# Optimization experiments

Hardware: AMD Instinct MI355X
Metric: run time of the kernel (lower is better)

## Reference

```python
import jax, jax.numpy as jnp
import numpy as np

B, S, F_IN = 128, 64, 32          # batch, window_size (seq), input features
E, L, H, HOR = 96, 4, 8, 24       # embed_dim, num_layers, num_heads, horizon
E2 = 2 * E                        # attention hidden size (conv output channels)
D = E2 // H                       # head_dim
FLAT = S * E2                     # flattened fc feature size


def _ln(x, scale, offset, eps=1e-5):
    mu = jnp.mean(x, axis=-1, keepdims=True)
    var = jnp.var(x, axis=-1, keepdims=True)
    return (x - mu) * jax.lax.rsqrt(var + eps) * scale + offset


def _gattention(h, qk_w, qk_b, mass_w, mass_b, v_w, v_b):
    b, s, _ = h.shape
    qk = (h @ qk_w + qk_b).reshape(b, s, H, D).transpose(0, 2, 1, 3)  # (b,h,s,d)
    # d^2 = |qi|^2 + |qj|^2 - 2 qi.qj  (GEMM identity; exact value is >= 0)
    sq = jnp.sum(qk * qk, axis=-1)                                    # (b,h,s)
    dot = jnp.einsum('bhid,bhjd->bhij', qk, qk)
    d2 = jnp.maximum(sq[:, :, :, None] + sq[:, :, None, :] - 2.0 * dot, 0.0) + 1e-6
    mass = jax.nn.softplus(h @ mass_w + mass_b).transpose(0, 2, 1)    # (b,h,s)
    scores = (mass[:, :, :, None] * mass[:, :, None, :]) / d2
    w = jax.nn.softmax(scores, axis=-1)
    v = (h @ v_w + v_b).reshape(b, s, H, D).transpose(0, 2, 1, 3)
    out = jnp.einsum('bhij,bhjd->bhid', w, v)
    return out.transpose(0, 2, 1, 3).reshape(b, s, E2)


def setup_inputs() -> dict:
    key = jax.random.key(0)
    ks = iter(jax.random.split(key, 16))
    r = lambda *shape: jax.random.normal(next(ks), shape, jnp.float32) * 0.02
    return dict(
        x=jax.random.normal(next(ks), (B, S, F_IN), jnp.float32),
        proj_w=r(F_IN, E), proj_b=jnp.zeros((E,), jnp.float32),
        ln0_s=jnp.ones((E,), jnp.float32), ln0_o=jnp.zeros((E,), jnp.float32),
        conv_w=r(4, 4, E, E2), conv_b=jnp.zeros((E2,), jnp.float32),
        ln1_s=jnp.ones((E2,), jnp.float32), ln1_o=jnp.zeros((E2,), jnp.float32),
        qk_w=r(L, E2, E2), qk_b=jnp.zeros((L, E2), jnp.float32),
        mass_w=r(L, E2, H), mass_b=jnp.zeros((L, H), jnp.float32),
        v_w=r(L, E2, E2), v_b=jnp.zeros((L, E2), jnp.float32),
        norm_s=jnp.ones((L, E2), jnp.float32), norm_o=jnp.zeros((L, E2), jnp.float32),
        mlp_w1=r(E2, 4 * E), mlp_b1=jnp.zeros((4 * E,), jnp.float32),
        mlp_w2=r(4 * E, E2), mlp_b2=jnp.zeros((E2,), jnp.float32),
        fc_w=r(FLAT, FLAT), fc_b=jnp.zeros((FLAT,), jnp.float32),
        ln2_s=jnp.ones((FLAT,), jnp.float32), ln2_o=jnp.zeros((FLAT,), jnp.float32),
        out_w=r(FLAT, HOR), out_b=jnp.zeros((HOR,), jnp.float32),
    )


def reference(x, proj_w, proj_b, ln0_s, ln0_o, conv_w, conv_b, ln1_s, ln1_o,
              qk_w, qk_b, mass_w, mass_b, v_w, v_b, norm_s, norm_o,
              mlp_w1, mlp_b1, mlp_w2, mlp_b2, fc_w, fc_b, ln2_s, ln2_o,
              out_w, out_b):
    # proj: Linear -> LN -> gelu
    h = jax.nn.gelu(_ln(x @ proj_w + proj_b, ln0_s, ln0_o))            # (B,S,E)
    # hk.Conv2D on rank-3 input: treated as a single unbatched HWC image
    y = jax.lax.conv_general_dilated(
        h[None], conv_w, window_strides=(1, 1), padding='SAME',
        dimension_numbers=('NHWC', 'HWIO', 'NHWC'))[0] + conv_b        # (B,S,E2)
    h = jax.nn.gelu(_ln(y, ln1_s, ln1_o))
    for i in range(L):
        a = _gattention(h, qk_w[i], qk_b[i], mass_w[i], mass_b[i], v_w[i], v_b[i])
        h = jax.nn.gelu(_ln(h + a, norm_s[i], norm_o[i]))
    h = h + (jax.nn.gelu(h @ mlp_w1 + mlp_b1) @ mlp_w2 + mlp_b2)
    f = _ln(jax.nn.gelu(h.reshape(B, FLAT) @ fc_w + fc_b), ln2_s, ln2_o)
    return f @ out_w + out_b                                           # (B,HOR)
```

## Files before the change

kernel.cpp:

```cpp
#include <hip/hip_runtime.h>
#include <math.h>

typedef __attribute__((ext_vector_type(8))) short short8;
typedef __attribute__((ext_vector_type(4))) float f32x4;

__device__ __forceinline__ unsigned short bf16_rne(float f) {
  union { float f; unsigned u; } x; x.f = f;
  unsigned r = x.u + 0x7FFFu + ((x.u >> 16) & 1u);
  return (unsigned short)(r >> 16);
}

__device__ __forceinline__ float gelu_f(float x) {
  float z = 0.7978845608028654f * (x + 0.044715f * x * x * x);
  z = fminf(fmaxf(z, -15.f), 15.f);
  float e = __expf(2.f * z);
  float th = (e - 1.f) / (e + 1.f);
  return 0.5f * x * (1.f + th);
}

__device__ __forceinline__ float softplus_f(float x) {
  return (x > 15.f) ? x : log1pf(__expf(x));
}

__device__ __forceinline__ float wave_sum(float v) {
  #pragma unroll
  for (int off = 32; off > 0; off >>= 1) v += __shfl_down(v, off, 64);
  return v;
}

__global__ __launch_bounds__(256) void pre_kern(
    const float* __restrict__ x, const float* __restrict__ w,
    const float* __restrict__ b, const float* __restrict__ s,
    const float* __restrict__ o, unsigned short* __restrict__ h0bf,
    const float* __restrict__ cw, unsigned short* __restrict__ cwT)
{
  if (blockIdx.x >= 2048) {
    int e = (blockIdx.x - 2048) * 256 + threadIdx.x;
    int co = e % 192, rest = e / 192;
    int ci = rest % 96, tap = rest / 96;
    cwT[((size_t)tap * 192 + co) * 96 + ci] = bf16_rne(cw[e]);
    return;
  }
  int t = threadIdx.x, wave = t >> 6, l = t & 63;
  size_t row = (size_t)blockIdx.x * 4 + wave;
  const float* xr = x + row * 32;
  bool has2 = (l < 32);
  int c1 = l, c2 = has2 ? 64 + l : 0;
  float v1 = b[c1], v2 = b[c2];
  #pragma unroll
  for (int k = 0; k < 32; ++k) {
    float xv = xr[k];
    v1 += xv * w[k * 96 + c1];
    v2 += xv * w[k * 96 + c2];
  }
  if (!has2) v2 = 0.f;
  float sum = wave_sum(v1 + v2);
  float ssq = wave_sum(v1 * v1 + v2 * v2);
  sum = __shfl(sum, 0, 64); ssq = __shfl(ssq, 0, 64);
  float mu = sum / 96.f, var = ssq / 96.f - mu * mu;
  float inv = rsqrtf(var + 1e-5f);
  float f1 = gelu_f((v1 - mu) * inv * s[c1] + o[c1]);
  h0bf[row * 96 + c1] = bf16_rne(f1);
  if (has2) {
    float f2 = gelu_f((v2 - mu) * inv * s[c2] + o[c2]);
    h0bf[row * 96 + c2] = bf16_rne(f2);
  }
}

__global__ __launch_bounds__(256) void conv_kern(
    const unsigned short* __restrict__ h0bf, const unsigned short* __restrict__ cwT,
    const float* __restrict__ cb, float* __restrict__ y)
{
  __shared__ unsigned short As[12 * 64 * 8];
  __shared__ unsigned short Ws[12 * 64 * 8];
  int t = threadIdx.x;
  int i = blockIdx.x;
  int n0 = blockIdx.y * 64;
  int wave = t >> 6, lane = t & 63, quad = lane >> 4, l16 = lane & 15;
  f32x4 zero4 = {0.f, 0.f, 0.f, 0.f};
  f32x4 acc[4];
  #pragma unroll
  for (int nt = 0; nt < 4; ++nt) acc[nt] = zero4;
  for (int tap = 0; tap < 16; ++tap) {
    int kh = tap >> 2, kw = tap & 3;
    int si = i + kh - 1;
    if (si < 0 || si >= 128) continue;
    {
      int j = t & 63, g = t >> 6;
      int sj = j + kw - 1;
      bool ok = (sj >= 0 && sj < 64);
      #pragma unroll
      for (int q = 0; q < 3; ++q) {
        int kb = g + 4 * q;
        short8 v = {0,0,0,0,0,0,0,0};
        if (ok) v = *(const short8*)(h0bf + (size_t)(si * 64 + sj) * 96 + kb * 8);
        *(short8*)(As + (kb * 64 + j) * 8) = v;
      }
    }
    {
      int n = t & 63, g = t >> 6;
      #pragma unroll
      for (int q = 0; q < 3; ++q) {
        int kb = g + 4 * q;
        *(short8*)(Ws + (kb * 64 + n) * 8) =
            *(const short8*)(cwT + ((size_t)tap * 192 + n0 + n) * 96 + kb * 8);
      }
    }
    __syncthreads();
    #pragma unroll
    for (int ks = 0; ks < 3; ++ks) {
      int kbq = ks * 4 + quad;
      short8 a = *(const short8*)(As + (kbq * 64 + wave * 16 + l16) * 8);
      #pragma unroll
      for (int nt = 0; nt < 4; ++nt) {
        short8 b = *(const short8*)(Ws + (kbq * 64 + nt * 16 + l16) * 8);
        acc[nt] = __builtin_amdgcn_mfma_f32_16x16x32_bf16(a, b, acc[nt], 0, 0, 0);
      }
    }
    __syncthreads();
  }
  #pragma unroll
  for (int nt = 0; nt < 4; ++nt) {
    int col = n0 + nt * 16 + l16;
    float bv = cb[col];
    #pragma unroll
    for (int r = 0; r < 4; ++r) {
      int row = wave * 16 + quad * 4 + r;
      y[(size_t)(i * 64 + row) * 192 + col] = acc[nt][r] + bv;
    }
  }
}

__global__ __launch_bounds__(256) void ln_act_kern(
    const float* __restrict__ y, const float* __restrict__ res,
    const float* __restrict__ s, const float* __restrict__ o,
    float* __restrict__ h32, unsigned short* __restrict__ hbf)
{
  int t = threadIdx.x, wave = t >> 6, l = t & 63;
  size_t base = ((size_t)blockIdx.x * 4 + wave) * 192;
  float v0 = y[base + l], v1 = y[base + 64 + l], v2 = y[base + 128 + l];
  if (res) { v0 += res[base + l]; v1 += res[base + 64 + l]; v2 += res[base + 128 + l]; }
  float sum = wave_sum(v0 + v1 + v2);
  float ssq = wave_sum(v0 * v0 + v1 * v1 + v2 * v2);
  sum = __shfl(sum, 0, 64); ssq = __shfl(ssq, 0, 64);
  float mu = sum * (1.f / 192.f);
  float var = ssq * (1.f / 192.f) - mu * mu;
  float inv = rsqrtf(var + 1e-5f);
  float f0 = gelu_f((v0 - mu) * inv * s[l] + o[l]);
  float f1 = gelu_f((v1 - mu) * inv * s[64 + l] + o[64 + l]);
  float f2 = gelu_f((v2 - mu) * inv * s[128 + l] + o[128 + l]);
  h32[base + l] = f0; h32[base + 64 + l] = f1; h32[base + 128 + l] = f2;
  hbf[base + l] = bf16_rne(f0); hbf[base + 64 + l] = bf16_rne(f1); hbf[base + 128 + l] = bf16_rne(f2);
}

__device__ __forceinline__ void stage_w(
    unsigned short* Wt, const float* qw, const float* vw, const float* mw,
    int half, int k0, int t)
{
  for (int c = t; c < 1664; c += 256) {
    int kb = c / 208, n = c - kb * 208;
    short8 v8;
    if (n < 192) {
      const float* src = (n < 96) ? (qw + half * 96 + n) : (vw + half * 96 + n - 96);
      #pragma unroll
      for (int jj = 0; jj < 8; ++jj)
        v8[jj] = (short)bf16_rne(src[(size_t)(k0 + kb * 8 + jj) * 192]);
    } else if (n < 196) {
      const float* src = mw + half * 4 + (n - 192);
      #pragma unroll
      for (int jj = 0; jj < 8; ++jj)
        v8[jj] = (short)bf16_rne(src[(size_t)(k0 + kb * 8 + jj) * 8]);
    } else {
      v8 = (short8){0,0,0,0,0,0,0,0};
    }
    *(short8*)(Wt + c * 8) = v8;
  }
}

__global__ __launch_bounds__(256) void layer_attn(
    const unsigned short* __restrict__ hbf,
    const float* __restrict__ qw, const float* __restrict__ qb,
    const float* __restrict__ vw, const float* __restrict__ vb,
    const float* __restrict__ mw, const float* __restrict__ mb,
    float* __restrict__ att)
{
  extern __shared__ char smem[];
  unsigned short* qk_lds = (unsigned short*)smem;
  unsigned short* v_ldsp = (unsigned short*)(smem + 16384);
  unsigned short* w_bfp  = (unsigned short*)(smem + 32768);
  float* mmp = (float*)(smem + 65536);
  float* sqp = (float*)(smem + 66560);
  unsigned short* A_bf = (unsigned short*)smem;
  unsigned short* Wt   = (unsigned short*)(smem + 24576);

  int t = threadIdx.x;
  int bb = blockIdx.x >> 1, half = blockIdx.x & 1;
  int wv = t >> 6, lane = t & 63, quad = lane >> 4, l16 = lane & 15;

  for (int c = t; c < 1536; c += 256) {
    int kb = c >> 6, m = c & 63;
    *(short8*)(A_bf + c * 8) =
        *(const short8*)(hbf + ((size_t)bb * 64 + m) * 192 + kb * 8);
  }
  stage_w(Wt, qw, vw, mw, half, 0, t);
  __syncthreads();
  f32x4 acc[13];
  #pragma unroll
  for (int i = 0; i < 13; ++i) acc[i] = (f32x4){0.f,0.f,0.f,0.f};
  for (int kt = 0; kt < 3; ++kt) {
    #pragma unroll
    for (int ks = 0; ks < 2; ++ks) {
      int kq = ks * 4 + quad;
      short8 a = *(const short8*)(A_bf + ((kt * 8 + kq) * 64 + wv * 16 + l16) * 8);
      #pragma unroll
      for (int nt = 0; nt < 13; ++nt) {
        short8 b = *(const short8*)(Wt + (kq * 208 + nt * 16 + l16) * 8);
        acc[nt] = __builtin_amdgcn_mfma_f32_16x16x32_bf16(a, b, acc[nt], 0, 0, 0);
      }
    }
    if (kt < 2) {
      __syncthreads();
      stage_w(Wt, qw, vw, mw, half, (kt + 1) * 64, t);
      __syncthreads();
    }
  }
  __syncthreads();

  {
    int zh = t >> 6, zs = t & 63;
    *(short8*)(qk_lds + ((zh * 4 + 3) * 64 + zs) * 8) = (short8){0,0,0,0,0,0,0,0};
  }
  int row = wv * 16 + quad * 4;
  #pragma unroll
  for (int nt = 0; nt < 6; ++nt) {
    int n = nt * 16 + l16;
    int hl = n / 24, d = n - hl * 24;
    float bqv = qb[half * 96 + n];
    #pragma unroll
    for (int r = 0; r < 4; ++r)
      qk_lds[((hl * 4 + (d >> 3)) * 64 + row + r) * 8 + (d & 7)] =
          bf16_rne(acc[nt][r] + bqv);
  }
  #pragma unroll
  for (int nt = 0; nt < 6; ++nt) {
    int n = nt * 16 + l16;
    int hl = n / 24, d = n - hl * 24;
    float bvv = vb[half * 96 + n];
    #pragma unroll
    for (int r = 0; r < 4; ++r) {
      int sidx = row + r;
      v_ldsp[((hl * 8 + (sidx >> 3)) * 32 + d) * 8 + (sidx & 7)] =
          bf16_rne(acc[nt + 6][r] + bvv);
    }
  }
  if (l16 < 4) {
    float mbv = mb[half * 4 + l16];
    #pragma unroll
    for (int r = 0; r < 4; ++r)
      mmp[(row + r) * 4 + l16] = softplus_f(acc[12][r] + mbv);
  }
  __syncthreads();

  const unsigned short* qh = qk_lds + (wv * 4) * 64 * 8;
  short8 frag[4];
  #pragma unroll
  for (int x2 = 0; x2 < 4; ++x2)
    frag[x2] = *(const short8*)(qh + (quad * 64 + x2 * 16 + l16) * 8);
  f32x4 s16[4][4];
  #pragma unroll
  for (int mt = 0; mt < 4; ++mt)
    #pragma unroll
    for (int nt = 0; nt < 4; ++nt)
      s16[mt][nt] = __builtin_amdgcn_mfma_f32_16x16x32_bf16(
          frag[mt], frag[nt], (f32x4){0.f,0.f,0.f,0.f}, 0, 0, 0);
  float* sqh = sqp + wv * 64;
  #pragma unroll
  for (int mt = 0; mt < 4; ++mt)
    #pragma unroll
    for (int r = 0; r < 4; ++r)
      if (l16 == quad * 4 + r) sqh[mt * 16 + l16] = s16[mt][mt][r];
  __syncthreads();
  f32x4 sqr[4], mr[4];
  float sqc[4], mc[4];
  #pragma unroll
  for (int mt = 0; mt < 4; ++mt) {
    sqr[mt] = *(const f32x4*)(sqh + mt * 16 + quad * 4);
    #pragma unroll
    for (int r = 0; r < 4; ++r) mr[mt][r] = mmp[(mt * 16 + quad * 4 + r) * 4 + wv];
  }
  #pragma unroll
  for (int nt = 0; nt < 4; ++nt) {
    sqc[nt] = sqh[nt * 16 + l16];
    mc[nt]  = mmp[(nt * 16 + l16) * 4 + wv];
  }
  #pragma unroll
  for (int mt = 0; mt < 4; ++mt)
    #pragma unroll
    for (int nt = 0; nt < 4; ++nt)
      #pragma unroll
      for (int r = 0; r < 4; ++r) {
        float d2 = fmaxf(sqr[mt][r] + sqc[nt] - 2.f * s16[mt][nt][r], 0.f) + 1e-6f;
        s16[mt][nt][r] = mr[mt][r] * mc[nt] / d2;
      }
  f32x4 inv4[4];
  #pragma unroll
  for (int mt = 0; mt < 4; ++mt)
    #pragma unroll
    for (int r = 0; r < 4; ++r) {
      float mx = fmaxf(fmaxf(s16[mt][0][r], s16[mt][1][r]),
                       fmaxf(s16[mt][2][r], s16[mt][3][r]));
      #pragma unroll
      for (int off = 1; off < 16; off <<= 1) mx = fmaxf(mx, __shfl_xor(mx, off, 64));
      float sm = 0.f;
      #pragma unroll
      for (int nt = 0; nt < 4; ++nt) {
        float e = __expf(s16[mt][nt][r] - mx);
        s16[mt][nt][r] = e;
        sm += e;
      }
      #pragma unroll
      for (int off = 1; off < 16; off <<= 1) sm += __shfl_xor(sm, off, 64);
      inv4[mt][r] = 1.f / sm;
    }

  unsigned short* wb = w_bfp + wv * (8 * 64 * 8);
  #pragma unroll
  for (int mt = 0; mt < 4; ++mt)
    #pragma unroll
    for (int nt = 0; nt < 4; ++nt)
      #pragma unroll
      for (int r = 0; r < 4; ++r) {
        int si = mt * 16 + quad * 4 + r, sj = nt * 16 + l16;
        wb[((sj >> 3) * 64 + si) * 8 + (sj & 7)] = bf16_rne(s16[mt][nt][r]);
      }
  __syncthreads();

  const unsigned short* vh = v_ldsp + wv * (8 * 32 * 8);
  f32x4 o2[4][2];
  #pragma unroll
  for (int mt = 0; mt < 4; ++mt)
    #pragma unroll
    for (int nt = 0; nt < 2; ++nt) o2[mt][nt] = (f32x4){0.f,0.f,0.f,0.f};
  #pragma unroll
  for (int ks = 0; ks < 2; ++ks) {
    int kq = ks * 4 + quad;
    short8 aw[4], bv2[2];
    #pragma unroll
    for (int mt = 0; mt < 4; ++mt)
      aw[mt] = *(const short8*)(wb + (kq * 64 + mt * 16 + l16) * 8);
    #pragma unroll
    for (int nt = 0; nt < 2; ++nt)
      bv2[nt] = *(const short8*)(vh + (kq * 32 + nt * 16 + l16) * 8);
    #pragma unroll
    for (int mt = 0; mt < 4; ++mt)
      #pragma unroll
      for (int nt = 0; nt < 2; ++nt)
        o2[mt][nt] = __builtin_amdgcn_mfma_f32_16x16x32_bf16(aw[mt], bv2[nt], o2[mt][nt], 0, 0, 0);
  }
  int hg = half * 4 + wv;
  size_t obase = ((size_t)bb * 64) * 192 + hg * 24;
  #pragma unroll
  for (int mt = 0; mt < 4; ++mt)
    #pragma unroll
    for (int nt = 0; nt < 2; ++nt) {
      int col = nt * 16 + l16;
      if (col < 24) {
        #pragma unroll
        for (int r = 0; r < 4; ++r) {
          int sidx = mt * 16 + quad * 4 + r;
          att[obase + (size_t)sidx * 192 + col] = o2[mt][nt][r] * inv4[mt][r];
        }
      }
    }
}

__global__ __launch_bounds__(256) void gemm_small(
    const unsigned short* __restrict__ A, int lda,
    const float* __restrict__ W, int ldw,
    const float* __restrict__ bias, const float* __restrict__ res,
    float* __restrict__ outF, unsigned short* __restrict__ outB,
    int K, int ldo, int act)
{
  __shared__ unsigned short As[8 * 64 * 8];
  __shared__ unsigned short Ws[8 * 64 * 8];
  int t = threadIdx.x;
  int m0 = blockIdx.x * 64, n0 = blockIdx.y * 64;
  int wave = t >> 6, lane = t & 63, quad = lane >> 4, l16 = lane & 15;
  f32x4 zero4 = {0.f, 0.f, 0.f, 0.f};
  f32x4 acc[4];
  #pragma unroll
  for (int nt = 0; nt < 4; ++nt) acc[nt] = zero4;
  for (int k0 = 0; k0 < K; k0 += 64) {
    {
      int kb = t & 7, m = t >> 3;
      #pragma unroll
      for (int r = 0; r < 2; ++r) {
        int mm = m + r * 32;
        *(short8*)(As + (kb * 64 + mm) * 8) =
            *(const short8*)(A + (size_t)(m0 + mm) * lda + k0 + kb * 8);
      }
    }
    {
      int n = t & 63, g = t >> 6;
      #pragma unroll
      for (int q = 0; q < 2; ++q) {
        int kb = g + 4 * q;
        short8 v;
        #pragma unroll
        for (int jj = 0; jj < 8; ++jj)
          v[jj] = (short)bf16_rne(W[(size_t)(k0 + kb * 8 + jj) * ldw + n0 + n]);
        *(short8*)(Ws + (kb * 64 + n) * 8) = v;
      }
    }
    __syncthreads();
    #pragma unroll
    for (int ks = 0; ks < 2; ++ks) {
      short8 a = *(const short8*)(As + ((ks * 4 + quad) * 64 + wave * 16 + l16) * 8);
      #pragma unroll
      for (int nt = 0; nt < 4; ++nt) {
        short8 b = *(const short8*)(Ws + ((ks * 4 + quad) * 64 + nt * 16 + l16) * 8);
        acc[nt] = __builtin_amdgcn_mfma_f32_16x16x32_bf16(a, b, acc[nt], 0, 0, 0);
      }
    }
    __syncthreads();
  }
  #pragma unroll
  for (int nt = 0; nt < 4; ++nt) {
    int col = n0 + nt * 16 + l16;
    float bv = bias[col];
    #pragma unroll
    for (int r = 0; r < 4; ++r) {
      int row = m0 + wave * 16 + quad * 4 + r;
      float v = acc[nt][r] + bv;
      if (act) v = gelu_f(v);
      if (res) v += res[(size_t)row * ldo + col];
      if (outF) outF[(size_t)row * ldo + col] = v;
      if (outB) outB[(size_t)row * ldo + col] = bf16_rne(v);
    }
  }
}

__global__ __launch_bounds__(256) void gemm_fc(
    const unsigned short* __restrict__ A, const float* __restrict__ W,
    float* __restrict__ part)
{
  __shared__ unsigned short As[8 * 128 * 8];
  __shared__ unsigned short Bs[8 * 64 * 8];
  int t = threadIdx.x;
  int n0 = blockIdx.x * 64;
  int split = blockIdx.y;
  int wave = t >> 6, lane = t & 63, quad = lane >> 4, l16 = lane & 15;
  int wm = wave * 32;
  int a_kb = t & 7, a_m = t >> 3;
  int w_n4 = t & 15, w_kr = t >> 4;
  f32x4 zero4 = {0.f, 0.f, 0.f, 0.f};
  f32x4 acc[2][4];
  #pragma unroll
  for (int mt = 0; mt < 2; ++mt)
    #pragma unroll
    for (int nt = 0; nt < 4; ++nt) acc[mt][nt] = zero4;
  int kk = split * 3072;
  short8 aR[4]; f32x4 wR[4];
  #pragma unroll
  for (int r = 0; r < 4; ++r)
    aR[r] = *(const short8*)(A + (size_t)(a_m + r * 32) * 12288 + kk + a_kb * 8);
  #pragma unroll
  for (int r = 0; r < 4; ++r)
    wR[r] = *(const f32x4*)(W + (size_t)(kk + w_kr + 16 * r) * 12288 + n0 + w_n4 * 4);
  for (int it = 0; it < 48; ++it) {
    #pragma unroll
    for (int r = 0; r < 4; ++r)
      *(short8*)(As + (a_kb * 128 + a_m + r * 32) * 8) = aR[r];
    #pragma unroll
    for (int r = 0; r < 4; ++r) {
      int k = w_kr + 16 * r, kb = k >> 3, kj = k & 7;
      #pragma unroll
      for (int j = 0; j < 4; ++j)
        Bs[(kb * 64 + w_n4 * 4 + j) * 8 + kj] = bf16_rne(wR[r][j]);
    }
    __syncthreads();
    if (it < 47) {
      int kn = kk + 64;
      #pragma unroll
      for (int r = 0; r < 4; ++r)
        aR[r] = *(const short8*)(A + (size_t)(a_m + r * 32) * 12288 + kn + a_kb * 8);
      #pragma unroll
      for (int r = 0; r < 4; ++r)
        wR[r] = *(const f32x4*)(W + (size_t)(kn + w_kr + 16 * r) * 12288 + n0 + w_n4 * 4);
    }
    #pragma unroll
    for (int ks = 0; ks < 2; ++ks) {
      int kq = ks * 4 + quad;
      short8 a[2], b[4];
      #pragma unroll
      for (int mt = 0; mt < 2; ++mt)
        a[mt] = *(const short8*)(As + (kq * 128 + wm + mt * 16 + l16) * 8);
      #pragma unroll
      for (int nt = 0; nt < 4; ++nt)
        b[nt] = *(const short8*)(Bs + (kq * 64 + nt * 16 + l16) * 8);
      #pragma unroll
      for (int mt = 0; mt < 2; ++mt)
        #pragma unroll
        for (int nt = 0; nt < 4; ++nt)
          acc[mt][nt] = __builtin_amdgcn_mfma_f32_16x16x32_bf16(a[mt], b[nt], acc[mt][nt], 0, 0, 0);
    }
    __syncthreads();
    kk += 64;
  }
  float* po = part + (size_t)split * 128 * 12288;
  #pragma unroll
  for (int mt = 0; mt < 2; ++mt) {
    #pragma unroll
    for (int nt = 0; nt < 4; ++nt) {
      int col = n0 + nt * 16 + l16;
      #pragma unroll
      for (int r = 0; r < 4; ++r) {
        int row = wm + mt * 16 + quad * 4 + r;
        po[(size_t)row * 12288 + col] = acc[mt][nt][r];
      }
    }
  }
}

__global__ __launch_bounds__(256) void final_kern(
    const float* __restrict__ part, const float* __restrict__ fb,
    const float* __restrict__ s, const float* __restrict__ o,
    const float* __restrict__ ow, const float* __restrict__ ob,
    float* __restrict__ out)
{
  __shared__ float gls[12288];
  __shared__ float a1[4], a2[4];
  __shared__ float red[4][24];
  int m = blockIdx.x, t = threadIdx.x;
  const f32x4* p0 = (const f32x4*)(part + (size_t)m * 12288);
  const size_t S4 = (size_t)128 * 12288 / 4;
  float s1 = 0.f, s2 = 0.f;
  for (int k4 = t; k4 < 3072; k4 += 256) {
    f32x4 v = p0[k4] + p0[k4 + S4] + p0[k4 + 2 * S4] + p0[k4 + 3 * S4];
    f32x4 bb = *(const f32x4*)(fb + k4 * 4);
    f32x4 g;
    #pragma unroll
    for (int c = 0; c < 4; ++c) g[c] = gelu_f(v[c] + bb[c]);
    *(f32x4*)(gls + k4 * 4) = g;
    s1 += g[0] + g[1] + g[2] + g[3];
    s2 += g[0]*g[0] + g[1]*g[1] + g[2]*g[2] + g[3]*g[3];
  }
  s1 = wave_sum(s1); s2 = wave_sum(s2);
  int wv = t >> 6, ln = t & 63;
  if (ln == 0) { a1[wv] = s1; a2[wv] = s2; }
  __syncthreads();
  float sum = a1[0] + a1[1] + a1[2] + a1[3];
  float ssq = a2[0] + a2[1] + a2[2] + a2[3];
  float mu = sum / 12288.f, var = ssq / 12288.f - mu * mu;
  float inv = rsqrtf(var + 1e-5f);
  f32x4 acc6[6];
  #pragma unroll
  for (int j = 0; j < 6; ++j) acc6[j] = (f32x4){0.f,0.f,0.f,0.f};
  for (int k = t; k < 12288; k += 256) {
    float f = (gls[k] - mu) * inv * s[k] + o[k];
    const f32x4* owr = (const f32x4*)(ow + (size_t)k * 24);
    #pragma unroll
    for (int j = 0; j < 6; ++j) acc6[j] += f * owr[j];
  }
  #pragma unroll
  for (int j = 0; j < 6; ++j)
    #pragma unroll
    for (int c = 0; c < 4; ++c) {
      float v = wave_sum(acc6[j][c]);
      if (ln == 0) red[wv][j * 4 + c] = v;
    }
  __syncthreads();
  if (t < 24) out[m * 24 + t] = red[0][t] + red[1][t] + red[2][t] + red[3][t] + ob[t];
}

extern "C" void kernel_launch(void* const* d_in, const int* in_sizes, int n_in,
                              void* d_out, int out_size, void* d_ws, size_t ws_size,
                              hipStream_t stream) {
  const float* x      = (const float*)d_in[0];
  const float* proj_w = (const float*)d_in[1];
  const float* proj_b = (const float*)d_in[2];
  const float* ln0_s  = (const float*)d_in[3];
  const float* ln0_o  = (const float*)d_in[4];
  const float* conv_w = (const float*)d_in[5];
  const float* conv_b = (const float*)d_in[6];
  const float* ln1_s  = (const float*)d_in[7];
  const float* ln1_o  = (const float*)d_in[8];
  const float* qk_w   = (const float*)d_in[9];
  const float* qk_b   = (const float*)d_in[10];
  const float* mass_w = (const float*)d_in[11];
  const float* mass_b = (const float*)d_in[12];
  const float* v_w    = (const float*)d_in[13];
  const float* v_b    = (const float*)d_in[14];
  const float* norm_s = (const float*)d_in[15];
  const float* norm_o = (const float*)d_in[16];
  const float* mlp_w1 = (const float*)d_in[17];
  const float* mlp_b1 = (const float*)d_in[18];
  const float* mlp_w2 = (const float*)d_in[19];
  const float* mlp_b2 = (const float*)d_in[20];
  const float* fc_w   = (const float*)d_in[21];
  const float* fc_b   = (const float*)d_in[22];
  const float* ln2_s  = (const float*)d_in[23];
  const float* ln2_o  = (const float*)d_in[24];
  const float* out_w  = (const float*)d_in[25];
  const float* out_b  = (const float*)d_in[26];
  float* out = (float*)d_out;

  char* ws = (char*)d_ws;
  unsigned short* h0bf = (unsigned short*)(ws + 0);
  float* h32           = (float*)(ws + 1572864);
  unsigned short* hbf  = (unsigned short*)(ws + 7864320);
  unsigned short* cwT  = (unsigned short*)(ws + 11010048);
  char* sc = ws + 11599872;
  float* t_att = (float*)(sc + 12582912);
  unsigned short* hid_bf = (unsigned short*)(sc + 18874368);
  float* partials = (float*)sc;

  pre_kern<<<3200, 256, 0, stream>>>(x, proj_w, proj_b, ln0_s, ln0_o, h0bf,
                                     conv_w, cwT);
  conv_kern<<<dim3(128, 3), 256, 0, stream>>>(h0bf, cwT, conv_b, t_att);
  ln_act_kern<<<2048, 256, 0, stream>>>(t_att, nullptr, ln1_s, ln1_o, h32, hbf);
  for (int l = 0; l < 4; ++l) {
    layer_attn<<<256, 256, 67584, stream>>>(hbf,
        qk_w + l * 36864, qk_b + l * 192,
        v_w + l * 36864, v_b + l * 192,
        mass_w + l * 1536, mass_b + l * 8, t_att);
    ln_act_kern<<<2048, 256, 0, stream>>>(t_att, h32, norm_s + l * 192,
                                          norm_o + l * 192, h32, hbf);
  }
  gemm_small<<<dim3(128, 6), 256, 0, stream>>>(hbf, 192, mlp_w1, 384, mlp_b1,
      nullptr, (float*)nullptr, hid_bf, 192, 384, 1);
  gemm_small<<<dim3(128, 3), 256, 0, stream>>>(hid_bf, 384, mlp_w2, 192, mlp_b2,
      h32, h32, hbf, 384, 192, 0);
  gemm_fc<<<dim3(192, 4), 256, 0, stream>>>(hbf, fc_w, partials);
  final_kern<<<128, 256, 0, stream>>>(partials, fc_b, ln2_s, ln2_o, out_w, out_b, out);
}
```

Baseline: 1.101 ms.

## Pre-convert weights to bf16, fuse LN into attention, double-buffer fc GEMM

Converts the QKV/mass, MLP1 and MLP2 weights once into pre-transposed bf16 layouts in pre_kern. This removes the repeated strided fp32 load and bf16 conversion done inside each attention block and each small GEMM. It folds the residual+LayerNorm+GELU of the previous layer into the start of the next attention kernel, which drops three ln_act launches, and ping-pongs the h32 and attention buffers. The attention kernel now stages the full K weight tile at once, which raises LDS use per block and may lower occupancy. The fc GEMM gains LDS double-buffering so the next tile is stored while the current one is computed.

Result: no change. 1.080 ms (-1.9%).

```diff
diff --git a/kernel.cpp b/kernel.cpp
--- a/kernel.cpp
+++ b/kernel.cpp
@@ -32,17 +32,58 @@
     const float* __restrict__ x, const float* __restrict__ w,
     const float* __restrict__ b, const float* __restrict__ s,
     const float* __restrict__ o, unsigned short* __restrict__ h0bf,
-    const float* __restrict__ cw, unsigned short* __restrict__ cwT)
+    const float* __restrict__ cw, unsigned short* __restrict__ cwT,
+    const float* __restrict__ qk_w, const float* __restrict__ v_w,
+    const float* __restrict__ mass_w, unsigned short* __restrict__ wqkvT,
+    const float* __restrict__ mlp_w1, unsigned short* __restrict__ wm1T,
+    const float* __restrict__ mlp_w2, unsigned short* __restrict__ wm2T)
 {
-  if (blockIdx.x >= 2048) {
-    int e = (blockIdx.x - 2048) * 256 + threadIdx.x;
-    int co = e % 192, rest = e / 192;
-    int ci = rest % 96, tap = rest / 96;
-    cwT[((size_t)tap * 192 + co) * 96 + ci] = bf16_rne(cw[e]);
-    return;
-  }
-  int t = threadIdx.x, wave = t >> 6, l = t & 63;
-  size_t row = (size_t)blockIdx.x * 4 + wave;
+  int t = threadIdx.x;
+  int bx = blockIdx.x;
+  if (bx >= 2048) {
+    bx -= 2048;
+    if (bx < 1152) {
+      int e = bx * 256 + t;
+      int co = e % 192, rest = e / 192;
+      int ci = rest % 96, tap = rest / 96;
+      cwT[((size_t)tap * 192 + co) * 96 + ci] = bf16_rne(cw[e]);
+      return;
+    }
+    bx -= 1152;
+    if (bx < 1248) {
+      int e = bx * 256 + t;
+      int jj = e & 7, s8 = e >> 3;
+      int n = s8 % 208, s9 = s8 / 208;
+      int kb = s9 % 24, s10 = s9 / 24;
+      int half = s10 & 1, l = s10 >> 1;
+      int k = kb * 8 + jj;
+      float v;
+      if (n < 96)       v = qk_w[(size_t)l * 36864 + (size_t)k * 192 + half * 96 + n];
+      else if (n < 192) v = v_w [(size_t)l * 36864 + (size_t)k * 192 + half * 96 + n - 96];
+      else if (n < 196) v = mass_w[(size_t)l * 1536 + (size_t)k * 8 + half * 4 + (n - 192)];
+      else v = 0.f;
+      wqkvT[e] = bf16_rne(v);
+      return;
+    }
+    bx -= 1248;
+    if (bx < 288) {
+      int e = bx * 256 + t;
+      int jj = e & 7, s8 = e >> 3;
+      int n = s8 % 384, kb = s8 / 384;
+      wm1T[e] = bf16_rne(mlp_w1[(size_t)(kb * 8 + jj) * 384 + n]);
+      return;
+    }
+    bx -= 288;
+    {
+      int e = bx * 256 + t;
+      int jj = e & 7, s8 = e >> 3;
+      int n = s8 % 192, kb = s8 / 192;
+      wm2T[e] = bf16_rne(mlp_w2[(size_t)(kb * 8 + jj) * 192 + n]);
+      return;
+    }
+  }
+  int wave = t >> 6, l = t & 63;
+  size_t row = (size_t)bx * 4 + wave;
   const float* xr = x + row * 32;
   bool has2 = (l < 32);
   int c1 = l, c2 = has2 ? 64 + l : 0;
@@ -153,75 +194,91 @@
   hbf[base + l] = bf16_rne(f0); hbf[base + 64 + l] = bf16_rne(f1); hbf[base + 128 + l] = bf16_rne(f2);
 }
 
-__device__ __forceinline__ void stage_w(
-    unsigned short* Wt, const float* qw, const float* vw, const float* mw,
-    int half, int k0, int t)
-{
-  for (int c = t; c < 1664; c += 256) {
-    int kb = c / 208, n = c - kb * 208;
-    short8 v8;
-    if (n < 192) {
-      const float* src = (n < 96) ? (qw + half * 96 + n) : (vw + half * 96 + n - 96);
-      #pragma unroll
-      for (int jj = 0; jj < 8; ++jj)
-        v8[jj] = (short)bf16_rne(src[(size_t)(k0 + kb * 8 + jj) * 192]);
-    } else if (n < 196) {
-      const float* src = mw + half * 4 + (n - 192);
-      #pragma unroll
-      for (int jj = 0; jj < 8; ++jj)
-        v8[jj] = (short)bf16_rne(src[(size_t)(k0 + kb * 8 + jj) * 8]);
-    } else {
-      v8 = (short8){0,0,0,0,0,0,0,0};
-    }
-    *(short8*)(Wt + c * 8) = v8;
-  }
-}
-
 __global__ __launch_bounds__(256) void layer_attn(
-    const unsigned short* __restrict__ hbf,
-    const float* __restrict__ qw, const float* __restrict__ qb,
-    const float* __restrict__ vw, const float* __restrict__ vb,
-    const float* __restrict__ mw, const float* __restrict__ mb,
-    float* __restrict__ att)
+    const unsigned short* __restrict__ hbf0,
+    const float* __restrict__ att_prev, const float* __restrict__ res_prev,
+    const float* __restrict__ ns, const float* __restrict__ no,
+    const unsigned short* __restrict__ wq,
+    const float* __restrict__ qb, const float* __restrict__ vb,
+    const float* __restrict__ mb,
+    float* __restrict__ h32_out, float* __restrict__ att)
 {
   extern __shared__ char smem[];
+  unsigned short* A_bf = (unsigned short*)smem;
+  unsigned short* Wt   = (unsigned short*)(smem + 24576);
   unsigned short* qk_lds = (unsigned short*)smem;
   unsigned short* v_ldsp = (unsigned short*)(smem + 16384);
   unsigned short* w_bfp  = (unsigned short*)(smem + 32768);
   float* mmp = (float*)(smem + 65536);
   float* sqp = (float*)(smem + 66560);
-  unsigned short* A_bf = (unsigned short*)smem;
-  unsigned short* Wt   = (unsigned short*)(smem + 24576);
 
   int t = threadIdx.x;
   int bb = blockIdx.x >> 1, half = blockIdx.x & 1;
   int wv = t >> 6, lane = t & 63, quad = lane >> 4, l16 = lane & 15;
 
-  for (int c = t; c < 1536; c += 256) {
-    int kb = c >> 6, m = c & 63;
-    *(short8*)(A_bf + c * 8) =
-        *(const short8*)(hbf + ((size_t)bb * 64 + m) * 192 + kb * 8);
-  }
-  stage_w(Wt, qw, vw, mw, half, 0, t);
+  if (att_prev) {
+    int r = t >> 2, q = t & 3;
+    size_t rbase = ((size_t)bb * 64 + r) * 192 + q * 48;
+    f32x4 yv[12];
+    float s1 = 0.f, s2 = 0.f;
+    #pragma unroll
+    for (int i = 0; i < 12; ++i) {
+      f32x4 a4 = *(const f32x4*)(att_prev + rbase + i * 4);
+      f32x4 r4 = *(const f32x4*)(res_prev + rbase + i * 4);
+      f32x4 yy = a4 + r4;
+      yv[i] = yy;
+      #pragma unroll
+      for (int c = 0; c < 4; ++c) { s1 += yy[c]; s2 += yy[c] * yy[c]; }
+    }
+    s1 += __shfl_xor(s1, 1, 64); s1 += __shfl_xor(s1, 2, 64);
+    s2 += __shfl_xor(s2, 1, 64); s2 += __shfl_xor(s2, 2, 64);
+    float mu = s1 * (1.f / 192.f);
+    float inv = rsqrtf(s2 * (1.f / 192.f) - mu * mu + 1e-5f);
+    #pragma unroll
+    for (int i = 0; i < 12; ++i) {
+      f32x4 sv = *(const f32x4*)(ns + q * 48 + i * 4);
+      f32x4 ov = *(const f32x4*)(no + q * 48 + i * 4);
+      f32x4 ff;
+      #pragma unroll
+      for (int c = 0; c < 4; ++c) ff[c] = gelu_f((yv[i][c] - mu) * inv * sv[c] + ov[c]);
+      *(f32x4*)(h32_out + rbase + i * 4) = ff;
+      yv[i] = ff;
+    }
+    #pragma unroll
+    for (int kb6 = 0; kb6 < 6; ++kb6) {
+      short8 v8;
+      #pragma unroll
+      for (int c = 0; c < 4; ++c) {
+        v8[c]     = (short)bf16_rne(yv[kb6 * 2][c]);
+        v8[4 + c] = (short)bf16_rne(yv[kb6 * 2 + 1][c]);
+      }
+      *(short8*)(A_bf + ((q * 6 + kb6) * 64 + r) * 8) = v8;
+    }
+  } else {
+    for (int c = t; c < 1536; c += 256) {
+      int kb = c >> 6, m = c & 63;
+      *(short8*)(A_bf + c * 8) =
+          *(const short8*)(hbf0 + ((size_t)bb * 64 + m) * 192 + kb * 8);
+    }
+  }
+  {
+    const unsigned short* wsrc = wq + (size_t)half * 39936;
+    for (int c = t; c < 4992; c += 256)
+      *(short8*)(Wt + c * 8) = *(const short8*)(wsrc + c * 8);
+  }
   __syncthreads();
+
   f32x4 acc[13];
   #pragma unroll
   for (int i = 0; i < 13; ++i) acc[i] = (f32x4){0.f,0.f,0.f,0.f};
-  for (int kt = 0; kt < 3; ++kt) {
-    #pragma unroll
-    for (int ks = 0; ks < 2; ++ks) {
-      int kq = ks * 4 + quad;
-      short8 a = *(const short8*)(A_bf + ((kt * 8 + kq) * 64 + wv * 16 + l16) * 8);
-      #pragma unroll
-      for (int nt = 0; nt < 13; ++nt) {
-        short8 b = *(const short8*)(Wt + (kq * 208 + nt * 16 + l16) * 8);
-        acc[nt] = __builtin_amdgcn_mfma_f32_16x16x32_bf16(a, b, acc[nt], 0, 0, 0);
-      }
-    }
-    if (kt < 2) {
-      __syncthreads();
-      stage_w(Wt, qw, vw, mw, half, (kt + 1) * 64, t);
-      __syncthreads();
+  #pragma unroll
+  for (int s = 0; s < 6; ++s) {
+    int kq = s * 4 + quad;
+    short8 a = *(const short8*)(A_bf + (kq * 64 + wv * 16 + l16) * 8);
+    #pragma unroll
+    for (int nt = 0; nt < 13; ++nt) {
+      short8 b = *(const short8*)(Wt + (kq * 208 + nt * 16 + l16) * 8);
+      acc[nt] = __builtin_amdgcn_mfma_f32_16x16x32_bf16(a, b, acc[nt], 0, 0, 0);
     }
   }
   __syncthreads();
@@ -374,9 +431,9 @@
     }
 }
 
-__global__ __launch_bounds__(256) void gemm_small(
+__global__ __launch_bounds__(256) void gemm_smallT(
     const unsigned short* __restrict__ A, int lda,
-    const float* __restrict__ W, int ldw,
+    const unsigned short* __restrict__ WT, int nld,
     const float* __restrict__ bias, const float* __restrict__ res,
     float* __restrict__ outF, unsigned short* __restrict__ outB,
     int K, int ldo, int act)
@@ -401,15 +458,13 @@
       }
     }
     {
-      int n = t & 63, g = t >> 6;
-      #pragma unroll
-      for (int q = 0; q < 2; ++q) {
-        int kb = g + 4 * q;
-        short8 v;
-        #pragma unroll
-        for (int jj = 0; jj < 8; ++jj)
-          v[jj] = (short)bf16_rne(W[(size_t)(k0 + kb * 8 + jj) * ldw + n0 + n]);
-        *(short8*)(Ws + (kb * 64 + n) * 8) = v;
+      int kbase = k0 >> 3;
+      #pragma unroll
+      for (int cc = 0; cc < 2; ++cc) {
+        int c = t + cc * 256;
+        int kb = c >> 6, nn = c & 63;
+        *(short8*)(Ws + c * 8) =
+            *(const short8*)(WT + ((size_t)(kbase + kb) * nld + n0 + nn) * 8);
       }
     }
     __syncthreads();
@@ -444,8 +499,8 @@
     const unsigned short* __restrict__ A, const float* __restrict__ W,
     float* __restrict__ part)
 {
-  __shared__ unsigned short As[8 * 128 * 8];
-  __shared__ unsigned short Bs[8 * 64 * 8];
+  __shared__ unsigned short As[2][8 * 128 * 8];
+  __shared__ unsigned short Bs[2][8 * 64 * 8];
   int t = threadIdx.x;
   int n0 = blockIdx.x * 64;
   int split = blockIdx.y;
@@ -467,20 +522,39 @@
   #pragma unroll
   for (int r = 0; r < 4; ++r)
     wR[r] = *(const f32x4*)(W + (size_t)(kk + w_kr + 16 * r) * 12288 + n0 + w_n4 * 4);
+  #pragma unroll
+  for (int r = 0; r < 4; ++r)
+    *(short8*)(As[0] + (a_kb * 128 + a_m + r * 32) * 8) = aR[r];
+  #pragma unroll
+  for (int r = 0; r < 4; ++r) {
+    int k = w_kr + 16 * r, kb = k >> 3, kj = k & 7;
+    #pragma unroll
+    for (int j = 0; j < 4; ++j)
+      Bs[0][(kb * 64 + w_n4 * 4 + j) * 8 + kj] = bf16_rne(wR[r][j]);
+  }
+  #pragma unroll
+  for (int r = 0; r < 4; ++r)
+    aR[r] = *(const short8*)(A + (size_t)(a_m + r * 32) * 12288 + kk + 64 + a_kb * 8);
+  #pragma unroll
+  for (int r = 0; r < 4; ++r)
+    wR[r] = *(const f32x4*)(W + (size_t)(kk + 64 + w_kr + 16 * r) * 12288 + n0 + w_n4 * 4);
+  __syncthreads();
   for (int it = 0; it < 48; ++it) {
-    #pragma unroll
-    for (int r = 0; r < 4; ++r)
-      *(short8*)(As + (a_kb * 128 + a_m + r * 32) * 8) = aR[r];
-    #pragma unroll
-    for (int r = 0; r < 4; ++r) {
-      int k = w_kr + 16 * r, kb = k >> 3, kj = k & 7;
-      #pragma unroll
-      for (int j = 0; j < 4; ++j)
-        Bs[(kb * 64 + w_n4 * 4 + j) * 8 + kj] = bf16_rne(wR[r][j]);
-    }
-    __syncthreads();
+    int buf = it & 1;
     if (it < 47) {
-      int kn = kk + 64;
+      #pragma unroll
+      for (int r = 0; r < 4; ++r)
+        *(short8*)(As[buf ^ 1] + (a_kb * 128 + a_m + r * 32) * 8) = aR[r];
+      #pragma unroll
+      for (int r = 0; r < 4; ++r) {
+        int k = w_kr + 16 * r, kb = k >> 3, kj = k & 7;
+        #pragma unroll
+        for (int j = 0; j < 4; ++j)
+          Bs[buf ^ 1][(kb * 64 + w_n4 * 4 + j) * 8 + kj] = bf16_rne(wR[r][j]);
+      }
+    }
+    if (it < 46) {
+      int kn = kk + (it + 2) * 64;
       #pragma unroll
       for (int r = 0; r < 4; ++r)
         aR[r] = *(const short8*)(A + (size_t)(a_m + r * 32) * 12288 + kn + a_kb * 8);
@@ -494,10 +568,10 @@
       short8 a[2], b[4];
       #pragma unroll
       for (int mt = 0; mt < 2; ++mt)
-        a[mt] = *(const short8*)(As + (kq * 128 + wm + mt * 16 + l16) * 8);
+        a[mt] = *(const short8*)(As[buf] + (kq * 128 + wm + mt * 16 + l16) * 8);
       #pragma unroll
       for (int nt = 0; nt < 4; ++nt)
-        b[nt] = *(const short8*)(Bs + (kq * 64 + nt * 16 + l16) * 8);
+        b[nt] = *(const short8*)(Bs[buf] + (kq * 64 + nt * 16 + l16) * 8);
       #pragma unroll
       for (int mt = 0; mt < 2; ++mt)
         #pragma unroll
@@ -505,7 +579,6 @@
           acc[mt][nt] = __builtin_amdgcn_mfma_f32_16x16x32_bf16(a[mt], b[nt], acc[mt][nt], 0, 0, 0);
     }
     __syncthreads();
-    kk += 64;
   }
   float* po = part + (size_t)split * 128 * 12288;
   #pragma unroll
@@ -606,31 +679,36 @@
   float* out = (float*)d_out;
 
   char* ws = (char*)d_ws;
-  unsigned short* h0bf = (unsigned short*)(ws + 0);
-  float* h32           = (float*)(ws + 1572864);
-  unsigned short* hbf  = (unsigned short*)(ws + 7864320);
-  unsigned short* cwT  = (unsigned short*)(ws + 11010048);
-  char* sc = ws + 11599872;
-  float* t_att = (float*)(sc + 12582912);
-  unsigned short* hid_bf = (unsigned short*)(sc + 18874368);
-  float* partials = (float*)sc;
-
-  pre_kern<<<3200, 256, 0, stream>>>(x, proj_w, proj_b, ln0_s, ln0_o, h0bf,
-                                     conv_w, cwT);
-  conv_kern<<<dim3(128, 3), 256, 0, stream>>>(h0bf, cwT, conv_b, t_att);
-  ln_act_kern<<<2048, 256, 0, stream>>>(t_att, nullptr, ln1_s, ln1_o, h32, hbf);
-  for (int l = 0; l < 4; ++l) {
-    layer_attn<<<256, 256, 67584, stream>>>(hbf,
-        qk_w + l * 36864, qk_b + l * 192,
-        v_w + l * 36864, v_b + l * 192,
-        mass_w + l * 1536, mass_b + l * 8, t_att);
-    ln_act_kern<<<2048, 256, 0, stream>>>(t_att, h32, norm_s + l * 192,
-                                          norm_o + l * 192, h32, hbf);
-  }
-  gemm_small<<<dim3(128, 6), 256, 0, stream>>>(hbf, 192, mlp_w1, 384, mlp_b1,
+  unsigned short* h0bf  = (unsigned short*)(ws + 0);
+  unsigned short* hbf   = (unsigned short*)(ws + 1572864);
+  unsigned short* cwT   = (unsigned short*)(ws + 4718592);
+  unsigned short* wqkvT = (unsigned short*)(ws + 5308416);
+  unsigned short* wm1T  = (unsigned short*)(ws + 5947392);
+  unsigned short* wm2T  = (unsigned short*)(ws + 6094848);
+  float* h32a = (float*)(ws + 6242304);
+  float* h32b = (float*)(ws + 12533760);
+  float* tA   = (float*)(ws + 18825216);
+  float* tB   = (float*)(ws + 25116672);
+  unsigned short* hid_bf = (unsigned short*)(ws + 31408128);
+  float* partials = (float*)(ws + 37699584);
+
+  pre_kern<<<5024, 256, 0, stream>>>(x, proj_w, proj_b, ln0_s, ln0_o, h0bf,
+      conv_w, cwT, qk_w, v_w, mass_w, wqkvT, mlp_w1, wm1T, mlp_w2, wm2T);
+  conv_kern<<<dim3(128, 3), 256, 0, stream>>>(h0bf, cwT, conv_b, tB);
+  ln_act_kern<<<2048, 256, 0, stream>>>(tB, nullptr, ln1_s, ln1_o, h32a, hbf);
+  layer_attn<<<256, 256, 104448, stream>>>(hbf, nullptr, nullptr, nullptr, nullptr,
+      wqkvT + 0 * 79872, qk_b + 0, v_b + 0, mass_b + 0, nullptr, tA);
+  layer_attn<<<256, 256, 104448, stream>>>(nullptr, tA, h32a, norm_s + 0, norm_o + 0,
+      wqkvT + 1 * 79872, qk_b + 192, v_b + 192, mass_b + 8, h32b, tB);
+  layer_attn<<<256, 256, 104448, stream>>>(nullptr, tB, h32b, norm_s + 192, norm_o + 192,
+      wqkvT + 2 * 79872, qk_b + 384, v_b + 384, mass_b + 16, h32a, tA);
+  layer_attn<<<256, 256, 104448, stream>>>(nullptr, tA, h32a, norm_s + 384, norm_o + 384,
+      wqkvT + 3 * 79872, qk_b + 576, v_b + 576, mass_b + 24, h32b, tB);
+  ln_act_kern<<<2048, 256, 0, stream>>>(tB, h32b, norm_s + 576, norm_o + 576, h32a, hbf);
+  gemm_smallT<<<dim3(128, 6), 256, 0, stream>>>(hbf, 192, wm1T, 384, mlp_b1,
       nullptr, (float*)nullptr, hid_bf, 192, 384, 1);
-  gemm_small<<<dim3(128, 3), 256, 0, stream>>>(hid_bf, 384, mlp_w2, 192, mlp_b2,
-      h32, h32, hbf, 384, 192, 0);
+  gemm_smallT<<<dim3(128, 3), 256, 0, stream>>>(hid_bf, 384, wm2T, 192, mlp_b2,
+      h32a, (float*)nullptr, hbf, 384, 192, 0);
   gemm_fc<<<dim3(192, 4), 256, 0, stream>>>(hbf, fc_w, partials);
   final_kern<<<128, 256, 0, stream>>>(partials, fc_b, ln2_s, ln2_o, out_w, out_b, out);
 }
```
